# Kernel optimization log

Hardware: AMD Instinct MI355X
Metric: run time of the kernel (lower is better)

Reference implementation:

```python
import jax, jax.numpy as jnp
import numpy as np

NQ = 10
C64 = jnp.complex64

# ---- gate matrices (built from traced fp32 params) ----

def u3(t, p, d):
    c = jnp.cos(t * 0.5).astype(C64)
    s = jnp.sin(t * 0.5).astype(C64)
    ep = jnp.exp(1j * p.astype(C64))
    ed = jnp.exp(1j * d.astype(C64))
    return jnp.stack([jnp.stack([c, -ed * s]), jnp.stack([ep * s, ep * ed * c])])

def ry(t):
    c = jnp.cos(t * 0.5).astype(C64)
    s = jnp.sin(t * 0.5).astype(C64)
    return jnp.stack([jnp.stack([c, -s]), jnp.stack([s, c])])

def rz(t):
    e = jnp.exp(-0.5j * t.astype(C64))
    ep = jnp.exp(0.5j * t.astype(C64))
    return jnp.diag(jnp.stack([e, ep]))

def rx(t):
    c = jnp.cos(t * 0.5).astype(C64)
    s = jnp.sin(t * 0.5).astype(C64)
    return jnp.stack([jnp.stack([c, -1j * s]), jnp.stack([-1j * s, c])])

def crz(t):
    one = jnp.ones((), C64)
    return jnp.diag(jnp.stack([one, one, jnp.exp(-0.5j * t.astype(C64)), jnp.exp(0.5j * t.astype(C64))]))

def crx(t):
    return jnp.eye(4, dtype=C64).at[2:, 2:].set(rx(t))

X = jnp.array([[0, 1], [1, 0]], dtype=C64)
CNOT = jnp.array([[1, 0, 0, 0], [0, 1, 0, 0], [0, 0, 0, 1], [0, 0, 1, 0]], dtype=C64)

# ---- gate application on state of shape (B, 2,...,2) ----

def ap1(st, U, w):
    ax = 1 + w
    s = jnp.moveaxis(st, ax, -1)
    s = s @ U.T
    return jnp.moveaxis(s, -1, ax)

def ap2(st, U, a, b):
    s = jnp.moveaxis(st, (1 + a, 1 + b), (-2, -1))
    sh = s.shape
    s = s.reshape(sh[:-2] + (4,)) @ U.T
    return jnp.moveaxis(s.reshape(sh), (-2, -1), (1 + a, 1 + b))

def conv_block(st, w, a, b):
    st = ap1(st, u3(w[0], w[1], w[2]), a)
    st = ap1(st, u3(w[3], w[4], w[5]), b)
    st = ap2(st, CNOT, a, b)
    st = ap1(st, ry(w[6]), a)
    st = ap1(st, rz(w[7]), b)
    st = ap2(st, CNOT, b, a)
    st = ap1(st, ry(w[8]), a)
    st = ap2(st, CNOT, a, b)
    st = ap1(st, u3(w[9], w[10], w[11]), a)
    st = ap1(st, u3(w[12], w[13], w[14]), b)
    return st

def pool_block(st, p, c, t):
    st = ap2(st, crz(p[0]), c, t)
    st = ap1(st, X, c)
    st = ap2(st, crx(p[1]), c, t)
    return st

def zexp(st, w):
    p = jnp.abs(st) ** 2  # fp32
    axes = tuple(ax for ax in range(1, NQ + 1) if ax != 1 + w)
    pz = p.sum(axis=axes)  # (B, 2)
    return pz[:, 0] - pz[:, 1]


def setup_inputs() -> dict:
    key = jax.random.key(0)
    ks = jax.random.split(key, 6)
    two_pi = 2.0 * np.pi
    return {
        "x": jax.random.normal(ks[0], (16384, 1024), dtype=jnp.float32),
        "weights_conv1": jax.random.uniform(ks[1], (10, 15), jnp.float32) * two_pi,
        "weights_conv2": jax.random.uniform(ks[2], (4, 15), jnp.float32) * two_pi,
        "weights_pool1": jax.random.uniform(ks[3], (5, 2), jnp.float32) * two_pi,
        "weights_pool2": jax.random.uniform(ks[4], (2, 2), jnp.float32) * two_pi,
        "weights_fc": jax.random.uniform(ks[5], (3,), jnp.float32) * two_pi,
    }


def reference(x, weights_conv1, weights_conv2, weights_pool1, weights_pool2, weights_fc):
    B = x.shape[0]
    # AmplitudeEmbedding with normalize=True (input already 1024-dim, no padding)
    nrm = jnp.linalg.norm(x, axis=1, keepdims=True)
    st = (x / nrm).astype(C64).reshape((B,) + (2,) * NQ)
    # conv layer 1: even pairs, odd pairs, wraparound (0, 9) reusing row 7
    for i in range(0, NQ, 2):
        st = conv_block(st, weights_conv1[i], i, i + 1)
    for i in range(1, NQ - 1, 2):
        st = conv_block(st, weights_conv1[i], i, i + 1)
    st = conv_block(st, weights_conv1[7], 0, NQ - 1)
    # pool layer 1
    for idx, i in enumerate(range(0, NQ, 2)):
        st = pool_block(st, weights_pool1[idx], i + 1, i)
    # conv layer 2 (stride-2 wires)
    for idx, i in enumerate(range(0, NQ - 2, 2)):
        st = conv_block(st, weights_conv2[idx], i, i + 2)
    # pool layer 2
    for idx, i in enumerate(range(0, NQ - 2, 4)):
        st = pool_block(st, weights_pool2[idx], i + 2, i)
    # fully-connected entanglers + RX rotations
    st = ap2(st, CNOT, 0, 4)
    st = ap2(st, CNOT, 2, 4)
    st = ap2(st, CNOT, 4, 0)
    st = ap1(st, rx(weights_fc[0]), 0)
    st = ap1(st, rx(weights_fc[1]), 2)
    st = ap1(st, rx(weights_fc[2]), 4)
    return jnp.stack([zexp(st, 0), zexp(st, 2)], axis=-1)  # (B, 2)
```

## Files before the change

### kernel.cpp

```cpp
#include <hip/hip_runtime.h>


typedef _Float16 f16;
typedef f16 f16x8 __attribute__((ext_vector_type(8)));
typedef f16 f16x4 __attribute__((ext_vector_type(4)));
typedef float f32x4 __attribute__((ext_vector_type(4)));

__device__ inline float2 cmul(float2 a, float2 b) {
    return make_float2(a.x * b.x - a.y * b.y, a.x * b.y + a.y * b.x);
}
__device__ inline float2 cadd(float2 a, float2 b) {
    return make_float2(a.x + b.x, a.y + b.y);
}

struct M2 { float2 m[4]; };

__device__ inline M2 m2_u3(float t, float p, float d) {
    float c = cosf(0.5f * t), s = sinf(0.5f * t);
    float2 ep = make_float2(cosf(p), sinf(p));
    float2 ed = make_float2(cosf(d), sinf(d));
    M2 U;
    U.m[0] = make_float2(c, 0.f);
    U.m[1] = make_float2(-ed.x * s, -ed.y * s);
    U.m[2] = make_float2(ep.x * s, ep.y * s);
    float2 epd = cmul(ep, ed);
    U.m[3] = make_float2(epd.x * c, epd.y * c);
    return U;
}
__device__ inline M2 m2_ry(float t) {
    float c = cosf(0.5f * t), s = sinf(0.5f * t);
    M2 U;
    U.m[0] = make_float2(c, 0.f);  U.m[1] = make_float2(-s, 0.f);
    U.m[2] = make_float2(s, 0.f);  U.m[3] = make_float2(c, 0.f);
    return U;
}
__device__ inline M2 m2_rz(float t) {
    float c = cosf(0.5f * t), s = sinf(0.5f * t);
    M2 U;
    U.m[0] = make_float2(c, -s); U.m[1] = make_float2(0.f, 0.f);
    U.m[2] = make_float2(0.f, 0.f); U.m[3] = make_float2(c, s);
    return U;
}
__device__ inline M2 m2_rx(float t) {
    float c = cosf(0.5f * t), s = sinf(0.5f * t);
    M2 U;
    U.m[0] = make_float2(c, 0.f);   U.m[1] = make_float2(0.f, -s);
    U.m[2] = make_float2(0.f, -s);  U.m[3] = make_float2(c, 0.f);
    return U;
}

__device__ inline void ap2x2(float2& x, float2& y, const M2& U) {
    float2 nx = cadd(cmul(U.m[0], x), cmul(U.m[1], y));
    float2 ny = cadd(cmul(U.m[2], x), cmul(U.m[3], y));
    x = nx; y = ny;
}
__device__ inline void apA(float2 v[4], const M2& U) { ap2x2(v[0], v[2], U); ap2x2(v[1], v[3], U); }
__device__ inline void apB(float2 v[4], const M2& U) { ap2x2(v[0], v[1], U); ap2x2(v[2], v[3], U); }
__device__ inline void swapv(float2& a, float2& b) { float2 t = a; a = b; b = t; }

__device__ inline void conv_col(const float* w, float2 v[4]) {
    apA(v, m2_u3(w[0], w[1], w[2]));
    apB(v, m2_u3(w[3], w[4], w[5]));
    swapv(v[2], v[3]);
    apA(v, m2_ry(w[6]));
    apB(v, m2_rz(w[7]));
    swapv(v[1], v[3]);
    apA(v, m2_ry(w[8]));
    swapv(v[2], v[3]);
    apA(v, m2_u3(w[9], w[10], w[11]));
    apB(v, m2_u3(w[12], w[13], w[14]));
}
__device__ inline void pool_col(const float* p, float2 v[4]) {
    {
        float c = cosf(0.5f * p[0]), s = sinf(0.5f * p[0]);
        v[2] = cmul(v[2], make_float2(c, -s));
        v[3] = cmul(v[3], make_float2(c, s));
    }
    swapv(v[0], v[2]); swapv(v[1], v[3]);
    {
        M2 U = m2_rx(p[1]);
        ap2x2(v[2], v[3], U);
    }
}

#define NORM_BLOCKS 2048

__global__ __launch_bounds__(256) void prep(const float* __restrict__ X,
                                            const float* __restrict__ wc1,
                                            const float* __restrict__ wc2,
                                            const float* __restrict__ wp1,
                                            const float* __restrict__ wp2,
                                            const float* __restrict__ wfc,
                                            float* __restrict__ nrm2,
                                            f16* __restrict__ Xh,
                                            f16* __restrict__ BTh) {
    __shared__ float2 st[2][1024];
    __shared__ float2 sm[27 * 16];
    __shared__ int2 sgp[27];
    const int bid = blockIdx.x;

    if (bid < NORM_BLOCKS) {
        const int w = threadIdx.x >> 6, l = threadIdx.x & 63;
#pragma unroll
        for (int r = 0; r < 2; r++) {
            const int row = bid * 8 + w * 2 + r;
            const float4* xr = (const float4*)(X + (size_t)row * 1024);
            float s = 0.f;
#pragma unroll
            for (int ch = 0; ch < 4; ch++) {
                float4 v = xr[ch * 64 + l];
                f16x4 h;
                h[0] = (f16)v.x; h[1] = (f16)v.y; h[2] = (f16)v.z; h[3] = (f16)v.w;
                *(f16x4*)(Xh + (size_t)row * 1024 + (ch * 64 + l) * 4) = h;
                s += v.x * v.x + v.y * v.y + v.z * v.z + v.w * v.w;
            }
#pragma unroll
            for (int off = 32; off >= 1; off >>= 1) s += __shfl_xor(s, off, 64);
            if (l == 0) nrm2[row] = s;
        }
        return;
    }

    const int t = bid - NORM_BLOCKS;

    {
        const int n = threadIdx.x >> 2, c = threadIdx.x & 3;
        if (n < 27) {
            float2 v[4];
            for (int i = 0; i < 4; i++) v[i] = make_float2(0.f, 0.f);
            v[c] = make_float2(1.f, 0.f);
            int a, b;
            if (n < 5)        { int i = 2*n;       a = i;   b = i+1; conv_col(wc1 + 15*i, v); }
            else if (n < 9)   { int i = 2*(n-5)+1; a = i;   b = i+1; conv_col(wc1 + 15*i, v); }
            else if (n == 9)  { a = 0; b = 9;      conv_col(wc1 + 105, v); }
            else if (n < 15)  { int idx = n-10, i = 2*idx; a = i+1; b = i; pool_col(wp1 + 2*idx, v); }
            else if (n < 19)  { int idx = n-15, i = 2*idx; a = i; b = i+2; conv_col(wc2 + 15*idx, v); }
            else if (n == 19) { a = 2; b = 0;      pool_col(wp2 + 0, v); }
            else if (n == 20) { a = 6; b = 4;      pool_col(wp2 + 2, v); }
            else if (n <= 23) {
                a = (n == 21) ? 0 : (n == 22) ? 2 : 4;
                b = (n == 23) ? 0 : 4;
                swapv(v[2], v[3]);
            } else {
                a = (n == 24) ? 0 : (n == 25) ? 2 : 4;
                b = a + 1;
                apA(v, m2_rx(wfc[n - 24]));
            }
            if (c == 0) sgp[n] = make_int2(9 - a, 9 - b);
            for (int i = 0; i < 4; i++) sm[n * 16 + i * 4 + c] = v[i];
        }
    }
    for (int i = threadIdx.x; i < 1024; i += 256)
        st[0][i] = make_float2(i == t ? 1.f : 0.f, 0.f);
    __syncthreads();

    int cur = 0;
    for (int g = 0; g < 27; g++) {
        const int2 p = sgp[g];
        const int p1 = p.x, p2 = p.y;
        const int lo = min(p1, p2), hi = max(p1, p2);
        const int q = threadIdx.x;
        const int m1 = (1 << lo) - 1;
        int tt = (q & m1) | ((q & ~m1) << 1);
        const int m2m = (1 << hi) - 1;
        const int i0 = (tt & m2m) | ((tt & ~m2m) << 1);
        int idx[4];
        for (int ga = 0; ga < 2; ga++)
            for (int gb = 0; gb < 2; gb++)
                idx[2 * ga + gb] = i0 | (ga << p1) | (gb << p2);
        float2 v[4];
        for (int i = 0; i < 4; i++) v[i] = st[cur][idx[i]];
        for (int i = 0; i < 4; i++) {
            float2 s = make_float2(0.f, 0.f);
            for (int j = 0; j < 4; j++) s = cadd(s, cmul(sm[g * 16 + i * 4 + j], v[j]));
            st[cur ^ 1][idx[i]] = s;
        }
        cur ^= 1;
        __syncthreads();
    }

    for (int s = threadIdx.x; s < 1024; s += 256) {
        const int b9 = (s >> 9) & 1, b7 = (s >> 7) & 1;
        if (b9 | b7) {
            const int grp = b9 ? b7 : 2;
            const int pos = (((s >> 8) & 1) << 7) | (s & 127);
            const int np = grp * 256 + pos;
            const float2 a = st[cur][s];
            BTh[(size_t)np * 1024 + t] = (f16)a.x;
            BTh[(size_t)(np + 768) * 1024 + t] = (f16)a.y;
        }
    }
}

__device__ __forceinline__ void glds16(const void* g, void* l) {
    __builtin_amdgcn_global_load_lds(
        (const __attribute__((address_space(1))) void*)g,
        (__attribute__((address_space(3))) void*)l, 16, 0, 0);
}

__global__ __launch_bounds__(256) void gemm_mfma(const f16* __restrict__ A,
                                                 const f16* __restrict__ Bt,
                                                 float* __restrict__ partial) {
    __shared__ char Ash[8192];
    __shared__ char Bsh[8192];
    __shared__ float pLDS[128][2][2];
    const int tid = threadIdx.x;
    const int l = tid & 63, w = tid >> 6;
    const int wr = w >> 1, wc = w & 1;
    const int row0 = blockIdx.x * 128, col0 = blockIdx.y * 128;

    const int mrow = l >> 2;
    const int kc = (l & 3) ^ ((l >> 3) & 3);
    const f16* aS0 = A  + (size_t)(row0 + 32 * w + mrow) * 1024 + kc * 8;
    const f16* aS1 = aS0 + 16 * 1024;
    const f16* bS0 = Bt + (size_t)(col0 + 32 * w + mrow) * 1024 + kc * 8;
    const f16* bS1 = bS0 + 16 * 1024;
    char* aD0 = Ash + 2048 * w;
    char* aD1 = aD0 + 1024;
    char* bD0 = Bsh + 2048 * w;
    char* bD1 = bD0 + 1024;

    int aOff[4], bOff[4];
#pragma unroll
    for (int i = 0; i < 4; i++) {
        int m = wr * 64 + i * 16 + (l & 15);
        aOff[i] = m * 64 + (((l >> 4) ^ ((m >> 1) & 3)) << 4);
        int n = wc * 64 + i * 16 + (l & 15);
        bOff[i] = n * 64 + (((l >> 4) ^ ((n >> 1) & 3)) << 4);
    }

    f32x4 acc[4][4];
    const f32x4 z = {0.f, 0.f, 0.f, 0.f};
#pragma unroll
    for (int i = 0; i < 4; i++)
#pragma unroll
        for (int j = 0; j < 4; j++) acc[i][j] = z;

    for (int k0 = 0; k0 < 1024; k0 += 32) {
        glds16(aS0 + k0, aD0);
        glds16(aS1 + k0, aD1);
        glds16(bS0 + k0, bD0);
        glds16(bS1 + k0, bD1);
        __syncthreads();
        f16x8 af[4], bf[4];
#pragma unroll
        for (int i = 0; i < 4; i++) {
            af[i] = *(const f16x8*)(Ash + aOff[i]);
            bf[i] = *(const f16x8*)(Bsh + bOff[i]);
        }
#pragma unroll
        for (int mi = 0; mi < 4; mi++)
#pragma unroll
            for (int ni = 0; ni < 4; ni++)
                acc[mi][ni] = __builtin_amdgcn_mfma_f32_16x16x32_f16(
                    af[mi], bf[ni], acc[mi][ni], 0, 0, 0);
        __syncthreads();
    }

    float c0[4][4], c1[4][4];
#pragma unroll
    for (int mi = 0; mi < 4; mi++)
#pragma unroll
        for (int rr = 0; rr < 4; rr++) { c0[mi][rr] = 0.f; c1[mi][rr] = 0.f; }
#pragma unroll
    for (int ni = 0; ni < 4; ni++) {
        const int n_glob = col0 + wc * 64 + ni * 16 + (l & 15);
        const int nm = (n_glob >= 768) ? n_glob - 768 : n_glob;
        const int grp = nm >> 8;
        const float w0 = (grp <= 1) ? 1.f : 0.f;
        const float w1 = (grp >= 1) ? 1.f : 0.f;
#pragma unroll
        for (int mi = 0; mi < 4; mi++)
#pragma unroll
            for (int rr = 0; rr < 4; rr++) {
                const float y = acc[mi][ni][rr];
                const float y2 = y * y;
                c0[mi][rr] += w0 * y2;
                c1[mi][rr] += w1 * y2;
            }
    }
#pragma unroll
    for (int off = 1; off < 16; off <<= 1)
#pragma unroll
        for (int mi = 0; mi < 4; mi++)
#pragma unroll
            for (int rr = 0; rr < 4; rr++) {
                c0[mi][rr] += __shfl_xor(c0[mi][rr], off, 64);
                c1[mi][rr] += __shfl_xor(c1[mi][rr], off, 64);
            }
    if ((l & 15) == 0) {
        const int q = l >> 4;
#pragma unroll
        for (int mi = 0; mi < 4; mi++)
#pragma unroll
            for (int rr = 0; rr < 4; rr++) {
                const int r = wr * 64 + mi * 16 + q * 4 + rr;
                pLDS[r][wc][0] = c0[mi][rr];
                pLDS[r][wc][1] = c1[mi][rr];
            }
    }
    __syncthreads();
    {
        const int r = tid >> 1, k = tid & 1;
        const float v = pLDS[r][0][k] + pLDS[r][1][k];
        partial[((size_t)blockIdx.y * 16384 + row0 + r) * 2 + k] = v;
    }
}

__global__ __launch_bounds__(256) void finalize(const float* __restrict__ partial,
                                                const float* __restrict__ nrm2,
                                                float* __restrict__ out) {
    const int i = blockIdx.x * 256 + threadIdx.x;
    const int b = i >> 1, k = i & 1;
    float s = 0.f;
#pragma unroll
    for (int ny = 0; ny < 12; ny++) s += partial[((size_t)ny * 16384 + b) * 2 + k];
    out[i] = 1.f - 2.f * s / nrm2[b];
}

extern "C" void kernel_launch(void* const* d_in, const int* in_sizes, int n_in,
                              void* d_out, int out_size, void* d_ws, size_t ws_size,
                              hipStream_t stream) {
    const float* x   = (const float*)d_in[0];
    const float* wc1 = (const float*)d_in[1];
    const float* wc2 = (const float*)d_in[2];
    const float* wp1 = (const float*)d_in[3];
    const float* wp2 = (const float*)d_in[4];
    const float* wfc = (const float*)d_in[5];
    float* out = (float*)d_out;

    uintptr_t wsp = (uintptr_t)d_ws;
    f16*    BTh    = (f16*)wsp;
    f16*    Xh     = (f16*)(wsp + (3u << 20));
    float*  nrm2   = (float*)(wsp + (35u << 20));
    float*  partial= (float*)(wsp + (35u << 20) + 65536);

    prep<<<NORM_BLOCKS + 1024, 256, 0, stream>>>(x, wc1, wc2, wp1, wp2, wfc, nrm2, Xh, BTh);
    gemm_mfma<<<dim3(128, 12), 256, 0, stream>>>(Xh, BTh, partial);
    finalize<<<128, 256, 0, stream>>>(partial, nrm2, out);
}
```

Baseline: 233.9 us.

## Hoist gate construction into separate kernel and simulate four basis columns per block

Gate matrices are now built once by a small single-block kernel and stored in workspace, so the 1024 simulation blocks no longer each recompute trig-heavy gate matrices. Each simulation block now propagates four basis states in place (256 blocks instead of 1024), reuses each gate matrix from registers across four states, and writes four adjacent f16 outputs as vector stores. Simulation blocks are placed first in the grid so they start before the norm blocks. The cost is an extra kernel launch, a larger shared-memory footprint per block, and fewer, longer simulation blocks.

```diff
diff --git a/kernel.cpp b/kernel.cpp
--- a/kernel.cpp
+++ b/kernel.cpp
@@ -83,27 +83,56 @@
     }
 }
 
+__global__ void build_gates(const float* wc1, const float* wc2,
+                            const float* wp1, const float* wp2,
+                            const float* wfc, int2* gp, float2* gm) {
+    const int t = threadIdx.x;
+    const int n = t >> 2, c = t & 3;
+    if (blockIdx.x != 0 || n >= 27) return;
+
+    float2 v[4];
+    for (int i = 0; i < 4; i++) v[i] = make_float2(0.f, 0.f);
+    v[c] = make_float2(1.f, 0.f);
+
+    int a, b;
+    if (n < 5)        { int i = 2*n;       a = i;   b = i+1; conv_col(wc1 + 15*i, v); }
+    else if (n < 9)   { int i = 2*(n-5)+1; a = i;   b = i+1; conv_col(wc1 + 15*i, v); }
+    else if (n == 9)  { a = 0; b = 9;      conv_col(wc1 + 105, v); }
+    else if (n < 15)  { int idx = n-10, i = 2*idx; a = i+1; b = i; pool_col(wp1 + 2*idx, v); }
+    else if (n < 19)  { int idx = n-15, i = 2*idx; a = i; b = i+2; conv_col(wc2 + 15*idx, v); }
+    else if (n == 19) { a = 2; b = 0;      pool_col(wp2 + 0, v); }
+    else if (n == 20) { a = 6; b = 4;      pool_col(wp2 + 2, v); }
+    else if (n <= 23) {
+        a = (n == 21) ? 0 : (n == 22) ? 2 : 4;
+        b = (n == 23) ? 0 : 4;
+        swapv(v[2], v[3]);
+    } else {
+        a = (n == 24) ? 0 : (n == 25) ? 2 : 4;
+        b = a + 1;
+        apA(v, m2_rx(wfc[n - 24]));
+    }
+    if (c == 0) gp[n] = make_int2(9 - a, 9 - b);
+    for (int i = 0; i < 4; i++) gm[n * 16 + i * 4 + c] = v[i];
+}
+
+#define SIM_BLOCKS 256
 #define NORM_BLOCKS 2048
 
 __global__ __launch_bounds__(256) void prep(const float* __restrict__ X,
-                                            const float* __restrict__ wc1,
-                                            const float* __restrict__ wc2,
-                                            const float* __restrict__ wp1,
-                                            const float* __restrict__ wp2,
-                                            const float* __restrict__ wfc,
+                                            const int2* __restrict__ gp,
+                                            const float2* __restrict__ gm,
                                             float* __restrict__ nrm2,
                                             f16* __restrict__ Xh,
                                             f16* __restrict__ BTh) {
-    __shared__ float2 st[2][1024];
-    __shared__ float2 sm[27 * 16];
-    __shared__ int2 sgp[27];
+    __shared__ float2 st[4][1025];
     const int bid = blockIdx.x;
 
-    if (bid < NORM_BLOCKS) {
+    if (bid >= SIM_BLOCKS) {
+        const int nb = bid - SIM_BLOCKS;
         const int w = threadIdx.x >> 6, l = threadIdx.x & 63;
 #pragma unroll
         for (int r = 0; r < 2; r++) {
-            const int row = bid * 8 + w * 2 + r;
+            const int row = nb * 8 + w * 2 + r;
             const float4* xr = (const float4*)(X + (size_t)row * 1024);
             float s = 0.f;
 #pragma unroll
@@ -121,42 +150,21 @@
         return;
     }
 
-    const int t = bid - NORM_BLOCKS;
-
-    {
-        const int n = threadIdx.x >> 2, c = threadIdx.x & 3;
-        if (n < 27) {
-            float2 v[4];
-            for (int i = 0; i < 4; i++) v[i] = make_float2(0.f, 0.f);
-            v[c] = make_float2(1.f, 0.f);
-            int a, b;
-            if (n < 5)        { int i = 2*n;       a = i;   b = i+1; conv_col(wc1 + 15*i, v); }
-            else if (n < 9)   { int i = 2*(n-5)+1; a = i;   b = i+1; conv_col(wc1 + 15*i, v); }
-            else if (n == 9)  { a = 0; b = 9;      conv_col(wc1 + 105, v); }
-            else if (n < 15)  { int idx = n-10, i = 2*idx; a = i+1; b = i; pool_col(wp1 + 2*idx, v); }
-            else if (n < 19)  { int idx = n-15, i = 2*idx; a = i; b = i+2; conv_col(wc2 + 15*idx, v); }
-            else if (n == 19) { a = 2; b = 0;      pool_col(wp2 + 0, v); }
-            else if (n == 20) { a = 6; b = 4;      pool_col(wp2 + 2, v); }
-            else if (n <= 23) {
-                a = (n == 21) ? 0 : (n == 22) ? 2 : 4;
-                b = (n == 23) ? 0 : 4;
-                swapv(v[2], v[3]);
-            } else {
-                a = (n == 24) ? 0 : (n == 25) ? 2 : 4;
-                b = a + 1;
-                apA(v, m2_rx(wfc[n - 24]));
-            }
-            if (c == 0) sgp[n] = make_int2(9 - a, 9 - b);
-            for (int i = 0; i < 4; i++) sm[n * 16 + i * 4 + c] = v[i];
-        }
-    }
-    for (int i = threadIdx.x; i < 1024; i += 256)
-        st[0][i] = make_float2(i == t ? 1.f : 0.f, 0.f);
+    const int sb = bid;
+    const int t0 = (((sb & 7) << 5) | (sb >> 3)) * 4;
+
+    for (int i = threadIdx.x; i < 1024; i += 256) {
+#pragma unroll
+        for (int c = 0; c < 4; c++)
+            st[c][i] = make_float2((i == t0 + c) ? 1.f : 0.f, 0.f);
+    }
     __syncthreads();
 
-    int cur = 0;
     for (int g = 0; g < 27; g++) {
-        const int2 p = sgp[g];
+        const int2 p = gp[g];
+        float2 m[16];
+#pragma unroll
+        for (int i = 0; i < 16; i++) m[i] = gm[g * 16 + i];
         const int p1 = p.x, p2 = p.y;
         const int lo = min(p1, p2), hi = max(p1, p2);
         const int q = threadIdx.x;
@@ -168,14 +176,19 @@
         for (int ga = 0; ga < 2; ga++)
             for (int gb = 0; gb < 2; gb++)
                 idx[2 * ga + gb] = i0 | (ga << p1) | (gb << p2);
-        float2 v[4];
-        for (int i = 0; i < 4; i++) v[i] = st[cur][idx[i]];
-        for (int i = 0; i < 4; i++) {
-            float2 s = make_float2(0.f, 0.f);
-            for (int j = 0; j < 4; j++) s = cadd(s, cmul(sm[g * 16 + i * 4 + j], v[j]));
-            st[cur ^ 1][idx[i]] = s;
+#pragma unroll
+        for (int c = 0; c < 4; c++) {
+            float2 v[4];
+#pragma unroll
+            for (int i = 0; i < 4; i++) v[i] = st[c][idx[i]];
+#pragma unroll
+            for (int i = 0; i < 4; i++) {
+                float2 s = make_float2(0.f, 0.f);
+#pragma unroll
+                for (int j = 0; j < 4; j++) s = cadd(s, cmul(m[i * 4 + j], v[j]));
+                st[c][idx[i]] = s;
+            }
         }
-        cur ^= 1;
         __syncthreads();
     }
 
@@ -185,9 +198,14 @@
             const int grp = b9 ? b7 : 2;
             const int pos = (((s >> 8) & 1) << 7) | (s & 127);
             const int np = grp * 256 + pos;
-            const float2 a = st[cur][s];
-            BTh[(size_t)np * 1024 + t] = (f16)a.x;
-            BTh[(size_t)(np + 768) * 1024 + t] = (f16)a.y;
+            f16x4 re, im;
+#pragma unroll
+            for (int c = 0; c < 4; c++) {
+                re[c] = (f16)st[c][s].x;
+                im[c] = (f16)st[c][s].y;
+            }
+            *(f16x4*)(BTh + (size_t)np * 1024 + t0) = re;
+            *(f16x4*)(BTh + (size_t)(np + 768) * 1024 + t0) = im;
         }
     }
 }
@@ -330,12 +348,15 @@
     float* out = (float*)d_out;
 
     uintptr_t wsp = (uintptr_t)d_ws;
-    f16*    BTh    = (f16*)wsp;
-    f16*    Xh     = (f16*)(wsp + (3u << 20));
-    float*  nrm2   = (float*)(wsp + (35u << 20));
-    float*  partial= (float*)(wsp + (35u << 20) + 65536);
-
-    prep<<<NORM_BLOCKS + 1024, 256, 0, stream>>>(x, wc1, wc2, wp1, wp2, wfc, nrm2, Xh, BTh);
+    int2*   gp     = (int2*)wsp;
+    float2* gm     = (float2*)(wsp + 1024);
+    f16*    BTh    = (f16*)(wsp + 8192);
+    f16*    Xh     = (f16*)(wsp + 8192 + (3u << 20));
+    float*  nrm2   = (float*)(wsp + 8192 + (35u << 20));
+    float*  partial= (float*)(wsp + 8192 + (35u << 20) + 65536);
+
+    build_gates<<<1, 128, 0, stream>>>(wc1, wc2, wp1, wp2, wfc, gp, gm);
+    prep<<<SIM_BLOCKS + NORM_BLOCKS, 256, 0, stream>>>(x, gp, gm, nrm2, Xh, BTh);
     gemm_mfma<<<dim3(128, 12), 256, 0, stream>>>(Xh, BTh, partial);
     finalize<<<128, 256, 0, stream>>>(partial, nrm2, out);
 }
```

After: 220.0 us. -6.0%, faster.
